# Kernel tuning notes

Hardware: AMD Instinct MI355X
Metric: run time of the kernel (lower is better)

Reference implementation:

```python
import jax, jax.numpy as jnp
import numpy as np

NUM_GROUPS, GROUP_SIZE, D_MODEL = 8, 4096, 1024
NUM_EXPERTS = 64
EXPERT_CAPACITY = 1024  # capacity_factor 2: 2 * total_tokens / num_experts


def setup_inputs() -> dict:
    key = jax.random.key(0)
    k1, k2, k3 = jax.random.split(key, 3)
    x = jax.random.normal(k1, (NUM_GROUPS, GROUP_SIZE, D_MODEL), dtype=jnp.float32)
    gate_kernel = jax.random.normal(k2, (D_MODEL, NUM_EXPERTS), dtype=jnp.float32) * 0.1
    gate_bias = jax.random.normal(k3, (NUM_EXPERTS,), dtype=jnp.float32) * 0.01
    temperature = jnp.ones((1,), dtype=jnp.float32)
    return {
        "x": x,
        "gate_kernel": gate_kernel,
        "gate_bias": gate_bias,
        "temperature": temperature,
        "expert_capacity": EXPERT_CAPACITY,
    }


def reference(x, gate_kernel, gate_bias, temperature, expert_capacity):
    # x: [G, S, D]; gate_kernel: [D, E]
    G, S, _ = x.shape
    E = gate_kernel.shape[1]

    router_logits = jnp.einsum("gsd,de->gse", x, gate_kernel) + gate_bias  # [G, S, E]
    safe_temp = jnp.maximum(temperature, 0.1)  # [1]
    router_probs = jax.nn.softmax(router_logits / safe_temp, axis=-1)  # [G, S, E]

    # Per-expert top-k over all flattened tokens.
    flat_probs = router_probs.transpose(2, 0, 1).reshape(E, G * S)  # [E, G*S]
    scores, token_indices = jax.lax.top_k(flat_probs, k=expert_capacity)  # [E, C]

    group_indices = token_indices // S  # [E, C]
    pos_indices = token_indices % S  # [E, C]
    expert_ids = jnp.broadcast_to(jnp.arange(E)[:, None], scores.shape)  # [E, C]

    # use_mask_routing=True path: scatter into capacity-limited dense masks.
    expert_masks = jnp.zeros((E, G, S), dtype=jnp.bool_).at[
        expert_ids, group_indices, pos_indices].set(True)
    weight_masks = jnp.zeros((E, G, S), dtype=x.dtype).at[
        expert_ids, group_indices, pos_indices].set(scores)

    loss = jnp.asarray(0.0, dtype=x.dtype)  # training=False
    return expert_masks, weight_masks, loss
```

## Files before the change

kernel.cpp:

```cpp
#include <hip/hip_runtime.h>
#include <math.h>

#define NG 8
#define SEQ 4096
#define DM 1024
#define NE 64
#define GS (NG * SEQ)
#define KSEL 1024
#define MASK_ELEMS (NE * GS)
#define SEG 16
#define SEGLEN (GS / SEG)
#define CAP 2048
#define CAP2 16384

typedef __attribute__((ext_vector_type(8))) short short8;
typedef __attribute__((ext_vector_type(4))) float f32x4;

__device__ __forceinline__ unsigned short f2bf(float v) {
  unsigned u = __float_as_uint(v);
  return (unsigned short)((u + 0x7FFFu + ((u >> 16) & 1u)) >> 16);
}
__device__ __forceinline__ float bf2f(unsigned short h) {
  return __uint_as_float(((unsigned)h) << 16);
}

#define GLDS(gsrc, ldst)                                                             \
  __builtin_amdgcn_global_load_lds(                                                  \
      (const __attribute__((address_space(1))) void*)(gsrc),                         \
      (__attribute__((address_space(3))) void*)(ldst), 16, 0, 0)

__global__ __launch_bounds__(256)
void k_split(const float* __restrict__ w, unsigned short* __restrict__ wph,
             unsigned short* __restrict__ wpm, unsigned* __restrict__ zbase) {
  const int t = blockIdx.x * 256 + threadIdx.x;
  if (t < NE * 256 + NE) zbase[t] = 0u;
  const int k = t >> 6, e = t & 63;
  float v = w[t];
  unsigned short h = f2bf(v); float r = v - bf2f(h);
  const int tile = k >> 5, g = (k >> 3) & 3, j = k & 7;
  const int cb = e >> 4, lrow = e & 15;
  const size_t o = (size_t)(tile * 4 + cb) * 512 + (g * 16 + lrow) * 8 + j;
  wph[o] = h; wpm[o] = f2bf(r);
}

__global__ __launch_bounds__(64)
void k_gemm_softmax(const float* __restrict__ x,
                    const unsigned short* __restrict__ wph,
                    const unsigned short* __restrict__ wpm,
                    const float* __restrict__ bias, const float* __restrict__ temp,
                    float* __restrict__ probsT) {
  __shared__ float S[8192];
  float (*Pt)[68] = (float (*)[68])S;
  float* Sf = S;

  const int lane = threadIdx.x;
  const int lrow = lane & 15, g = lane >> 4;
  const int m0 = blockIdx.x * 64;

  int irow[4], jcol[4];
  {
    union { unsigned short u[8]; short8 v; } ar, on;
#pragma unroll
    for (int j = 0; j < 8; ++j) { ar.u[j] = f2bf((float)lrow); on.u[j] = 0x3F80u; }
    f32x4 z = {0.f, 0.f, 0.f, 0.f};
    f32x4 p1 = __builtin_amdgcn_mfma_f32_16x16x32_bf16(ar.v, on.v, z, 0, 0, 0);
    f32x4 p2 = __builtin_amdgcn_mfma_f32_16x16x32_bf16(on.v, ar.v, z, 0, 0, 0);
#pragma unroll
    for (int b = 0; b < 4; ++b) {
      irow[b] = ((int)p1[b]) >> 5;
      jcol[b] = ((int)p2[b]) >> 5;
    }
  }

  f32x4 acc[4][4];
#pragma unroll
  for (int rf = 0; rf < 4; ++rf)
#pragma unroll
    for (int cb = 0; cb < 4; ++cb) acc[rf][cb] = (f32x4){0.f, 0.f, 0.f, 0.f};

#define ISSUE(T, buf)                                                                \
  {                                                                                  \
    _Pragma("unroll")                                                                \
    for (int q = 0; q < 8; ++q) {                                                    \
      const int c = q * 64 + lane;                                                   \
      const int gg = c >> 7, row = (c >> 1) & 63, half = c & 1;                      \
      const float* gsrc = x + (size_t)(m0 + row) * DM + (T) * 32 + gg * 8 + half * 4;\
      GLDS(gsrc, Sf + (buf) * 4096 + q * 256);                                       \
    }                                                                                \
    _Pragma("unroll")                                                                \
    for (int q = 0; q < 8; ++q) {                                                    \
      const unsigned short* bp = (q < 4) ? wph : wpm;                                \
      const unsigned short* gsrc = bp + (size_t)((T) * 4 + (q & 3)) * 512 + lane * 8;\
      GLDS(gsrc, Sf + (buf) * 4096 + 2048 + q * 256);                                \
    }                                                                                \
  }

#define COMPUTE(buf)                                                                 \
  {                                                                                  \
    const unsigned short* bb = (const unsigned short*)(Sf + (buf) * 4096 + 2048);    \
    _Pragma("unroll")                                                                \
    for (int rf = 0; rf < 4; ++rf) {                                                 \
      const float* ab = Sf + (buf) * 4096 + g * 512 + (rf * 16 + lrow) * 8;          \
      f32x4 lo = *(const f32x4*)ab;                                                  \
      f32x4 hi = *(const f32x4*)(ab + 4);                                            \
      union { unsigned short u[8]; short8 v; } ah, am;                               \
      _Pragma("unroll")                                                              \
      for (int j = 0; j < 8; ++j) {                                                  \
        float v0 = (j < 4) ? lo[j] : hi[j - 4];                                      \
        unsigned short h_ = f2bf(v0);                                                \
        ah.u[j] = h_; am.u[j] = f2bf(v0 - bf2f(h_));                                 \
      }                                                                              \
      _Pragma("unroll")                                                              \
      for (int cb = 0; cb < 4; ++cb) {                                               \
        short8 bh_ = *(const short8*)(bb + cb * 512 + lane * 8);                     \
        short8 bm_ = *(const short8*)(bb + 2048 + cb * 512 + lane * 8);              \
        acc[rf][cb] = __builtin_amdgcn_mfma_f32_16x16x32_bf16(ah.v, bh_,             \
                                                              acc[rf][cb], 0, 0, 0); \
        acc[rf][cb] = __builtin_amdgcn_mfma_f32_16x16x32_bf16(am.v, bh_,             \
                                                              acc[rf][cb], 0, 0, 0); \
        acc[rf][cb] = __builtin_amdgcn_mfma_f32_16x16x32_bf16(ah.v, bm_,             \
                                                              acc[rf][cb], 0, 0, 0); \
      }                                                                              \
    }                                                                                \
  }

#define WAIT16 { asm volatile("s_waitcnt vmcnt(16)" ::: "memory");                   \
                 __builtin_amdgcn_sched_barrier(0); }
#define WAIT0  { asm volatile("s_waitcnt vmcnt(0)" ::: "memory");                    \
                 __builtin_amdgcn_sched_barrier(0); }

  ISSUE(0, 0);
  ISSUE(1, 1);
  for (int t = 0; t < 30; ++t) {
    WAIT16;
    COMPUTE(t & 1);
    __builtin_amdgcn_sched_barrier(0);
    ISSUE(t + 2, t & 1);
  }
  WAIT16; COMPUTE(0);
  WAIT0;  COMPUTE(1);

#undef ISSUE
#undef COMPUTE
#undef WAIT16
#undef WAIT0

  {
    float st = temp[0];
    if (st < 0.1f) st = 0.1f;
    const float inv_t = 1.0f / st;
#pragma unroll
    for (int rf = 0; rf < 4; ++rf) {
#pragma unroll
      for (int b = 0; b < 4; ++b) {
        float l[4];
        float mx = -1.0e30f;
#pragma unroll
        for (int cb = 0; cb < 4; ++cb) {
          l[cb] = (acc[rf][cb][b] + bias[cb * 16 + jcol[b]]) * inv_t;
          mx = fmaxf(mx, l[cb]);
        }
        mx = fmaxf(mx, __shfl_xor(mx, 1));
        mx = fmaxf(mx, __shfl_xor(mx, 2));
        mx = fmaxf(mx, __shfl_xor(mx, 4));
        mx = fmaxf(mx, __shfl_xor(mx, 8));
        float p[4], s = 0.0f;
#pragma unroll
        for (int cb = 0; cb < 4; ++cb) { p[cb] = __expf(l[cb] - mx); s += p[cb]; }
        s += __shfl_xor(s, 1);
        s += __shfl_xor(s, 2);
        s += __shfl_xor(s, 4);
        s += __shfl_xor(s, 8);
        const float invs = 1.0f / s;
#pragma unroll
        for (int cb = 0; cb < 4; ++cb)
          Pt[cb * 16 + jcol[b]][rf * 16 + irow[b]] = p[cb] * invs;
      }
    }
  }

#pragma unroll
  for (int it = 0; it < 16; ++it) {
    const int e = it * 4 + (lane >> 4);
    const int tok = (lane & 15) * 4;
    *(float4*)(probsT + (size_t)e * GS + m0 + tok) = *(const float4*)(&Pt[e][tok]);
  }
}

__device__ __forceinline__ void pick_scan(const unsigned* __restrict__ bins,
                                          unsigned r_in, unsigned& bucket,
                                          unsigned& r_out, unsigned* res) {
  __syncthreads();
  const int tid = threadIdx.x;
  if (tid < 64) {
    uint4 b = ((const uint4*)bins)[tid];
    unsigned s3 = b.w, s2 = b.z + s3, s1 = b.y + s2, s0 = b.x + s1;
    unsigned suf = s0;
#pragma unroll
    for (int off = 1; off < 64; off <<= 1) {
      unsigned t = __shfl_down(suf, off);
      if (tid + off < 64) suf += t;
    }
    unsigned above = suf - s0;
    unsigned inc0 = above + s0, inc1 = above + s1, inc2 = above + s2, inc3 = above + s3;
    if (inc3 >= r_in && inc3 - b.w < r_in) { res[0] = 4 * tid + 3; res[1] = r_in - (inc3 - b.w); }
    if (inc2 >= r_in && inc2 - b.z < r_in) { res[0] = 4 * tid + 2; res[1] = r_in - (inc2 - b.z); }
    if (inc1 >= r_in && inc1 - b.y < r_in) { res[0] = 4 * tid + 1; res[1] = r_in - (inc1 - b.y); }
    if (inc0 >= r_in && inc0 - b.x < r_in) { res[0] = 4 * tid + 0; res[1] = r_in - (inc0 - b.x); }
  }
  __syncthreads();
  bucket = res[0];
  r_out = res[1];
}

__global__ __launch_bounds__(256)
void k_hist0(const float* __restrict__ probsT, unsigned* __restrict__ ghist0) {
  __shared__ unsigned h[4][256];
  const int tid = threadIdx.x, wv = tid >> 6;
  const int e = blockIdx.x >> 4;
  const int seg = blockIdx.x & (SEG - 1);
  h[0][tid] = 0; h[1][tid] = 0; h[2][tid] = 0; h[3][tid] = 0;
  __syncthreads();
  const float4* col = (const float4*)(probsT + (size_t)e * GS + seg * SEGLEN);
#pragma unroll
  for (int i = 0; i < SEGLEN / 1024; ++i) {
    float4 v = col[i * 256 + tid];
    atomicAdd(&h[wv][__float_as_uint(v.x) >> 24], 1u);
    atomicAdd(&h[wv][__float_as_uint(v.y) >> 24], 1u);
    atomicAdd(&h[wv][__float_as_uint(v.z) >> 24], 1u);
    atomicAdd(&h[wv][__float_as_uint(v.w) >> 24], 1u);
  }
  __syncthreads();
  unsigned c = h[0][tid] + h[1][tid] + h[2][tid] + h[3][tid];
  if (c) atomicAdd(&ghist0[e * 256 + tid], c);
}

__global__ __launch_bounds__(256)
void k_compact(const float* __restrict__ probsT, const unsigned* __restrict__ ghist0,
               unsigned* __restrict__ cCnt, int* __restrict__ cIdx,
               float* __restrict__ cKey) {
  __shared__ unsigned res[2];
  __shared__ unsigned locN, basePos;
  __shared__ int locIdx[2048];
  __shared__ float locKey[2048];
  const int tid = threadIdx.x;
  const int e = blockIdx.x >> 4;
  const int seg = blockIdx.x & (SEG - 1);

  if (tid == 0) locN = 0u;
  unsigned b0, r0;
  pick_scan(ghist0 + e * 256, KSEL, b0, r0, res);
  const unsigned blo = (b0 == 0u) ? 0u : (b0 - 1u);

  const float* col = probsT + (size_t)e * GS + seg * SEGLEN;
  for (int i = 0; i < SEGLEN / 256; ++i) {
    const int t = i * 256 + tid;
    const float p = col[t];
    if ((__float_as_uint(p) >> 24) >= blo) {
      unsigned pos = atomicAdd(&locN, 1u);
      locIdx[pos] = seg * SEGLEN + t;
      locKey[pos] = p;
    }
  }
  __syncthreads();
  if (tid == 0) basePos = locN ? atomicAdd(&cCnt[e], locN) : 0u;
  __syncthreads();
  const unsigned n = locN, bp = basePos;
  for (unsigned i = tid; i < n; i += 256) {
    const unsigned gp = bp + i;
    if (gp < CAP2) {
      cIdx[(size_t)e * CAP2 + gp] = locIdx[i];
      cKey[(size_t)e * CAP2 + gp] = locKey[i];
    }
  }
}

__global__ __launch_bounds__(256)
void k_select2(const unsigned* __restrict__ ghist0, const unsigned* __restrict__ cCnt,
               const int* __restrict__ cIdx, const float* __restrict__ cKey,
               const float* __restrict__ temp, unsigned* __restrict__ defCnt,
               unsigned* __restrict__ candCnt, int* __restrict__ candIdx,
               float* __restrict__ thrHiA) {
  __shared__ unsigned res[2];
  __shared__ unsigned h[4][256];
  __shared__ unsigned hs[256];
  __shared__ unsigned nd, nc;
  const int tid = threadIdx.x, wv = tid >> 6;
  const int e = blockIdx.x;
  const int cnt = (int)min(cCnt[e], (unsigned)CAP2);

  unsigned b0, r;
  pick_scan(ghist0 + e * 256, KSEL, b0, r, res);
  unsigned pfx = b0 << 24;

  for (int pass = 1; pass < 4; ++pass) {
    const int shift = 24 - 8 * pass;
    const unsigned hm = 0xFFFFFFFFu << (shift + 8);
    for (int i = tid; i < 1024; i += 256) ((unsigned*)h)[i] = 0u;
    __syncthreads();
    for (int i = tid; i < cnt; i += 256) {
      unsigned key = __float_as_uint(cKey[(size_t)e * CAP2 + i]);
      if ((key & hm) == (pfx & hm)) atomicAdd(&h[wv][(key >> shift) & 255], 1u);
    }
    __syncthreads();
    hs[tid] = h[0][tid] + h[1][tid] + h[2][tid] + h[3][tid];
    unsigned b, rn;
    pick_scan(hs, r, b, rn, res);
    pfx |= b << shift;
    r = rn;
  }

  const float thrv = __uint_as_float(pfx);
  float st = temp[0];
  if (st < 0.1f) st = 0.1f;
  const float rel = 2.0e-3f / st;
  const float hi = thrv * (1.0f + rel);
  const float lo = thrv * (1.0f - rel);
  if (tid == 0) thrHiA[e] = hi;

  if (tid == 0) { nd = 0u; nc = 0u; }
  __syncthreads();
  for (int i = tid; i < cnt; i += 256) {
    const float p = cKey[(size_t)e * CAP2 + i];
    const int t = cIdx[(size_t)e * CAP2 + i];
    if (p > hi) {
      atomicAdd(&nd, 1u);
    } else if (p >= lo) {
      unsigned pos = atomicAdd(&nc, 1u);
      if (pos < CAP) candIdx[e * CAP + pos] = t;
    }
  }
  __syncthreads();
  if (tid == 0) {
    defCnt[e] = nd;
    candCnt[e] = min(nc, (unsigned)CAP);
  }
}

__global__ __launch_bounds__(256)
void k_repair(const float* __restrict__ x, const float* __restrict__ w,
              const float* __restrict__ bias, const float* __restrict__ temp,
              const unsigned* __restrict__ candCnt, const int* __restrict__ candIdx,
              double* __restrict__ candKey) {
  __shared__ double red[4][64];
  const int e = blockIdx.x >> 4;
  const int chunk = blockIdx.x & 15;
  const int tid = threadIdx.x;
  const int ee = tid & 63, q = tid >> 6;
  const int cnt = (int)min(candCnt[e], (unsigned)CAP);

  double st = (double)temp[0];
  if (st < 0.1) st = 0.1;
  const double inv_t = 1.0 / st;

  for (int i = chunk; i < cnt; i += 16) {
    const int t = candIdx[e * CAP + i];
    const float* xr = x + (size_t)t * DM;
    double s0 = 0.0, s1 = 0.0, s2 = 0.0, s3 = 0.0;
    const int kb = q * 256;
    for (int k = kb; k < kb + 256; k += 4) {
      s0 += (double)xr[k + 0] * (double)w[(size_t)(k + 0) * NE + ee];
      s1 += (double)xr[k + 1] * (double)w[(size_t)(k + 1) * NE + ee];
      s2 += (double)xr[k + 2] * (double)w[(size_t)(k + 2) * NE + ee];
      s3 += (double)xr[k + 3] * (double)w[(size_t)(k + 3) * NE + ee];
    }
    red[q][ee] = (s0 + s1) + (s2 + s3);
    __syncthreads();
    if (tid < 64) {
      double l = (red[0][tid] + red[1][tid] + red[2][tid] + red[3][tid] +
                  (double)bias[tid]) * inv_t;
      double m = l;
#pragma unroll
      for (int off = 1; off < 64; off <<= 1) m = fmax(m, __shfl_xor(m, off));
      double ex = exp(l - m);
      double ss = ex;
#pragma unroll
      for (int off = 1; off < 64; off <<= 1) ss += __shfl_xor(ss, off);
      if (tid == e) candKey[e * CAP + i] = ex / ss;
    }
    __syncthreads();
  }
}

__global__ __launch_bounds__(256)
void k_scatter(const float* __restrict__ probsT, const float* __restrict__ thrHiA,
               float* __restrict__ out) {
  const int gid = blockIdx.x * 256 + threadIdx.x;
  const int base = gid * 4;
  const int e = base >> 15;
  float4 p = *(const float4*)(probsT + (size_t)base);
  const float hi = thrHiA[e];
  float pv[4] = {p.x, p.y, p.z, p.w};
  float mk[4], wt[4];
#pragma unroll
  for (int c = 0; c < 4; ++c) {
    bool sel = pv[c] > hi;
    mk[c] = sel ? 1.0f : 0.0f;
    wt[c] = sel ? pv[c] : 0.0f;
  }
  *(float4*)(out + (size_t)base) = make_float4(mk[0], mk[1], mk[2], mk[3]);
  *(float4*)(out + (size_t)MASK_ELEMS + base) = make_float4(wt[0], wt[1], wt[2], wt[3]);
  if (gid == 0) out[2 * (size_t)MASK_ELEMS] = 0.0f;
}

__global__ __launch_bounds__(256)
void k_finish(const unsigned* __restrict__ defCnt, const unsigned* __restrict__ candCnt,
              const int* __restrict__ candIdx, const double* __restrict__ candKey,
              const float* __restrict__ probsT, float* __restrict__ out) {
  __shared__ double kd[CAP];
  __shared__ int ti[CAP];
  const int e = blockIdx.x, tid = threadIdx.x;
  const int cnt = (int)min(candCnt[e], (unsigned)CAP);
  const int need = KSEL - (int)defCnt[e];

  for (int i = tid; i < cnt; i += 256) {
    kd[i] = candKey[e * CAP + i];
    ti[i] = candIdx[e * CAP + i];
  }
  __syncthreads();
  for (int i = tid; i < cnt; i += 256) {
    const double ki = kd[i];
    const int tii = ti[i];
    int rank = 0;
    for (int j = 0; j < cnt; ++j)
      rank += (kd[j] > ki) || (kd[j] == ki && ti[j] < tii);
    if (rank < need) {
      out[(size_t)e * GS + tii] = 1.0f;
      out[(size_t)MASK_ELEMS + (size_t)e * GS + tii] = probsT[(size_t)e * GS + tii];
    }
  }
}

extern "C" void kernel_launch(void* const* d_in, const int* in_sizes, int n_in,
                              void* d_out, int out_size, void* d_ws, size_t ws_size,
                              hipStream_t stream) {
  const float* x    = (const float*)d_in[0];
  const float* gw   = (const float*)d_in[1];
  const float* gb   = (const float*)d_in[2];
  const float* temp = (const float*)d_in[3];

  float* probsT    = (float*)d_ws;
  unsigned* ghist0 = (unsigned*)((char*)d_ws + (size_t)MASK_ELEMS * 4);
  unsigned* cCnt   = ghist0 + NE * 256;
  unsigned* defCnt = cCnt + NE;
  unsigned* candCnt = defCnt + NE;
  float* thrHiA    = (float*)(candCnt + NE);
  int* candIdx     = (int*)(thrHiA + NE);
  double* candKey  = (double*)(candIdx + NE * CAP);
  int* cIdx        = (int*)(candKey + NE * CAP);
  float* cKey      = (float*)(cIdx + (size_t)NE * CAP2);
  unsigned short* wph = (unsigned short*)(cKey + (size_t)NE * CAP2);
  unsigned short* wpm = wph + DM * NE;

  k_split<<<DM * NE / 256, 256, 0, stream>>>(gw, wph, wpm, ghist0);
  k_gemm_softmax<<<GS / 64, 64, 0, stream>>>(x, wph, wpm, gb, temp, probsT);
  k_hist0<<<NE * SEG, 256, 0, stream>>>(probsT, ghist0);
  k_compact<<<NE * SEG, 256, 0, stream>>>(probsT, ghist0, cCnt, cIdx, cKey);
  k_select2<<<NE, 256, 0, stream>>>(ghist0, cCnt, cIdx, cKey, temp, defCnt,
                                    candCnt, candIdx, thrHiA);
  k_repair<<<NE * 16, 256, 0, stream>>>(x, gw, gb, temp, candCnt, candIdx, candKey);
  k_scatter<<<MASK_ELEMS / 1024, 256, 0, stream>>>(probsT, thrHiA, (float*)d_out);
  k_finish<<<NE, 256, 0, stream>>>(defCnt, candCnt, candIdx, candKey,
                                   probsT, (float*)d_out);
}
```

Measured before the change: 112.4 us.

## Split GEMM-softmax block across four waves with XOR-swizzled K=64 staging

The router GEMM+softmax kernel moves from one 64-thread wave per 64-token block to four waves. Each wave now owns 16 rows and the cooperative loads stage a 64-wide K slice per step, which halves the pipeline iterations. The A tile in LDS uses an XOR swizzle to avoid bank conflicts, and the write-out of the transposed probabilities is shared across all 256 threads. In exchange it adds block barriers each step and doubles LDS use per block, which may reduce occupancy.

Result: faster. 92.59 us (-17.6%).

```diff
diff --git a/kernel.cpp b/kernel.cpp
--- a/kernel.cpp
+++ b/kernel.cpp
@@ -43,19 +43,21 @@
   wph[o] = h; wpm[o] = f2bf(r);
 }
 
-__global__ __launch_bounds__(64)
+__global__ __launch_bounds__(256, 2)
 void k_gemm_softmax(const float* __restrict__ x,
                     const unsigned short* __restrict__ wph,
                     const unsigned short* __restrict__ wpm,
                     const float* __restrict__ bias, const float* __restrict__ temp,
                     float* __restrict__ probsT) {
-  __shared__ float S[8192];
+  __shared__ float S[16384];
   float (*Pt)[68] = (float (*)[68])S;
-  float* Sf = S;
-
-  const int lane = threadIdx.x;
+
+  const int tid = threadIdx.x;
+  const int w = tid >> 6, lane = tid & 63;
   const int lrow = lane & 15, g = lane >> 4;
   const int m0 = blockIdx.x * 64;
+  const int arow_g = tid >> 4;
+  const int agr = (tid & 15) ^ (arow_g & 15);
 
   int irow[4], jcol[4];
   {
@@ -72,37 +74,34 @@
     }
   }
 
-  f32x4 acc[4][4];
-#pragma unroll
-  for (int rf = 0; rf < 4; ++rf)
-#pragma unroll
-    for (int cb = 0; cb < 4; ++cb) acc[rf][cb] = (f32x4){0.f, 0.f, 0.f, 0.f};
-
-#define ISSUE(T, buf)                                                                \
+  f32x4 acc[4];
+#pragma unroll
+  for (int cb = 0; cb < 4; ++cb) acc[cb] = (f32x4){0.f, 0.f, 0.f, 0.f};
+
+#define ISSUE(s, buf)                                                                \
   {                                                                                  \
     _Pragma("unroll")                                                                \
-    for (int q = 0; q < 8; ++q) {                                                    \
-      const int c = q * 64 + lane;                                                   \
-      const int gg = c >> 7, row = (c >> 1) & 63, half = c & 1;                      \
-      const float* gsrc = x + (size_t)(m0 + row) * DM + (T) * 32 + gg * 8 + half * 4;\
-      GLDS(gsrc, Sf + (buf) * 4096 + q * 256);                                       \
-    }                                                                                \
+    for (int c = 0; c < 4; ++c)                                                      \
+      GLDS(x + (size_t)(m0 + c * 16 + arow_g) * DM + (s) * 64 + agr * 4,             \
+           S + (buf) * 8192 + (c * 256 + tid) * 4);                                  \
     _Pragma("unroll")                                                                \
-    for (int q = 0; q < 8; ++q) {                                                    \
-      const unsigned short* bp = (q < 4) ? wph : wpm;                                \
-      const unsigned short* gsrc = bp + (size_t)((T) * 4 + (q & 3)) * 512 + lane * 8;\
-      GLDS(gsrc, Sf + (buf) * 4096 + 2048 + q * 256);                                \
-    }                                                                                \
+    for (int p = 0; p < 2; ++p)                                                      \
+      _Pragma("unroll")                                                              \
+      for (int c = 0; c < 2; ++c)                                                    \
+        GLDS((p ? wpm : wph) + (size_t)(s) * 4096 + c * 2048 + tid * 8,              \
+             S + (buf) * 8192 + 4096 + p * 2048 + c * 1024 + tid * 4);               \
   }
 
 #define COMPUTE(buf)                                                                 \
   {                                                                                  \
-    const unsigned short* bb = (const unsigned short*)(Sf + (buf) * 4096 + 2048);    \
+    const float* Af = S + (buf) * 8192;                                              \
+    const unsigned short* Bb = (const unsigned short*)(S + (buf) * 8192 + 4096);     \
     _Pragma("unroll")                                                                \
-    for (int rf = 0; rf < 4; ++rf) {                                                 \
-      const float* ab = Sf + (buf) * 4096 + g * 512 + (rf * 16 + lrow) * 8;          \
-      f32x4 lo = *(const f32x4*)ab;                                                  \
-      f32x4 hi = *(const f32x4*)(ab + 4);                                            \
+    for (int kt = 0; kt < 2; ++kt) {                                                 \
+      f32x4 lo = *(const f32x4*)(Af + (w * 16 + lrow) * 64 +                         \
+                                 ((kt * 8 + g * 2 + 0) ^ lrow) * 4);                 \
+      f32x4 hi = *(const f32x4*)(Af + (w * 16 + lrow) * 64 +                         \
+                                 ((kt * 8 + g * 2 + 1) ^ lrow) * 4);                 \
       union { unsigned short u[8]; short8 v; } ah, am;                               \
       _Pragma("unroll")                                                              \
       for (int j = 0; j < 8; ++j) {                                                  \
@@ -112,37 +111,38 @@
       }                                                                              \
       _Pragma("unroll")                                                              \
       for (int cb = 0; cb < 4; ++cb) {                                               \
-        short8 bh_ = *(const short8*)(bb + cb * 512 + lane * 8);                     \
-        short8 bm_ = *(const short8*)(bb + 2048 + cb * 512 + lane * 8);              \
-        acc[rf][cb] = __builtin_amdgcn_mfma_f32_16x16x32_bf16(ah.v, bh_,             \
-                                                              acc[rf][cb], 0, 0, 0); \
-        acc[rf][cb] = __builtin_amdgcn_mfma_f32_16x16x32_bf16(am.v, bh_,             \
-                                                              acc[rf][cb], 0, 0, 0); \
-        acc[rf][cb] = __builtin_amdgcn_mfma_f32_16x16x32_bf16(ah.v, bm_,             \
-                                                              acc[rf][cb], 0, 0, 0); \
+        short8 bh_ = *(const short8*)(Bb + (kt * 4 + cb) * 512 + lane * 8);          \
+        short8 bm_ = *(const short8*)(Bb + 4096 + (kt * 4 + cb) * 512 + lane * 8);   \
+        acc[cb] = __builtin_amdgcn_mfma_f32_16x16x32_bf16(ah.v, bh_, acc[cb], 0, 0, 0); \
+        acc[cb] = __builtin_amdgcn_mfma_f32_16x16x32_bf16(am.v, bh_, acc[cb], 0, 0, 0); \
+        acc[cb] = __builtin_amdgcn_mfma_f32_16x16x32_bf16(ah.v, bm_, acc[cb], 0, 0, 0); \
       }                                                                              \
     }                                                                                \
   }
 
-#define WAIT16 { asm volatile("s_waitcnt vmcnt(16)" ::: "memory");                   \
-                 __builtin_amdgcn_sched_barrier(0); }
-#define WAIT0  { asm volatile("s_waitcnt vmcnt(0)" ::: "memory");                    \
-                 __builtin_amdgcn_sched_barrier(0); }
+#define WAIT8 { asm volatile("s_waitcnt vmcnt(8)" ::: "memory");                     \
+                __builtin_amdgcn_sched_barrier(0); }
+#define WAIT0 { asm volatile("s_waitcnt vmcnt(0)" ::: "memory");                     \
+                __builtin_amdgcn_sched_barrier(0); }
 
   ISSUE(0, 0);
   ISSUE(1, 1);
-  for (int t = 0; t < 30; ++t) {
-    WAIT16;
-    COMPUTE(t & 1);
-    __builtin_amdgcn_sched_barrier(0);
-    ISSUE(t + 2, t & 1);
-  }
-  WAIT16; COMPUTE(0);
-  WAIT0;  COMPUTE(1);
+#pragma unroll
+  for (int s = 0; s < 14; ++s) {
+    WAIT8;
+    __builtin_amdgcn_s_barrier();
+    if (s & 1) { COMPUTE(1); } else { COMPUTE(0); }
+    __builtin_amdgcn_s_barrier();
+    ISSUE(s + 2, s & 1);
+  }
+  WAIT8; __builtin_amdgcn_s_barrier(); COMPUTE(0);
+  __builtin_amdgcn_s_barrier();
+  WAIT0; __builtin_amdgcn_s_barrier(); COMPUTE(1);
+  __syncthreads();
 
 #undef ISSUE
 #undef COMPUTE
-#undef WAIT16
+#undef WAIT8
 #undef WAIT0
 
   {
@@ -150,40 +150,39 @@
     if (st < 0.1f) st = 0.1f;
     const float inv_t = 1.0f / st;
 #pragma unroll
-    for (int rf = 0; rf < 4; ++rf) {
-#pragma unroll
-      for (int b = 0; b < 4; ++b) {
-        float l[4];
-        float mx = -1.0e30f;
-#pragma unroll
-        for (int cb = 0; cb < 4; ++cb) {
-          l[cb] = (acc[rf][cb][b] + bias[cb * 16 + jcol[b]]) * inv_t;
-          mx = fmaxf(mx, l[cb]);
-        }
-        mx = fmaxf(mx, __shfl_xor(mx, 1));
-        mx = fmaxf(mx, __shfl_xor(mx, 2));
-        mx = fmaxf(mx, __shfl_xor(mx, 4));
-        mx = fmaxf(mx, __shfl_xor(mx, 8));
-        float p[4], s = 0.0f;
-#pragma unroll
-        for (int cb = 0; cb < 4; ++cb) { p[cb] = __expf(l[cb] - mx); s += p[cb]; }
-        s += __shfl_xor(s, 1);
-        s += __shfl_xor(s, 2);
-        s += __shfl_xor(s, 4);
-        s += __shfl_xor(s, 8);
-        const float invs = 1.0f / s;
-#pragma unroll
-        for (int cb = 0; cb < 4; ++cb)
-          Pt[cb * 16 + jcol[b]][rf * 16 + irow[b]] = p[cb] * invs;
+    for (int b = 0; b < 4; ++b) {
+      float l[4];
+      float mx = -1.0e30f;
+#pragma unroll
+      for (int cb = 0; cb < 4; ++cb) {
+        l[cb] = (acc[cb][b] + bias[cb * 16 + jcol[b]]) * inv_t;
+        mx = fmaxf(mx, l[cb]);
       }
-    }
-  }
-
-#pragma unroll
-  for (int it = 0; it < 16; ++it) {
-    const int e = it * 4 + (lane >> 4);
-    const int tok = (lane & 15) * 4;
-    *(float4*)(probsT + (size_t)e * GS + m0 + tok) = *(const float4*)(&Pt[e][tok]);
+      mx = fmaxf(mx, __shfl_xor(mx, 1));
+      mx = fmaxf(mx, __shfl_xor(mx, 2));
+      mx = fmaxf(mx, __shfl_xor(mx, 4));
+      mx = fmaxf(mx, __shfl_xor(mx, 8));
+      float p[4], sm = 0.0f;
+#pragma unroll
+      for (int cb = 0; cb < 4; ++cb) { p[cb] = __expf(l[cb] - mx); sm += p[cb]; }
+      sm += __shfl_xor(sm, 1);
+      sm += __shfl_xor(sm, 2);
+      sm += __shfl_xor(sm, 4);
+      sm += __shfl_xor(sm, 8);
+      const float invs = 1.0f / sm;
+#pragma unroll
+      for (int cb = 0; cb < 4; ++cb)
+        Pt[cb * 16 + jcol[b]][w * 16 + irow[b]] = p[cb] * invs;
+    }
+  }
+  __syncthreads();
+
+  {
+    const int e = tid >> 2, qq = tid & 3;
+    float* dst = probsT + (size_t)e * GS + m0 + qq * 16;
+#pragma unroll
+    for (int c2 = 0; c2 < 4; ++c2)
+      *(float4*)(dst + c2 * 4) = *(const float4*)(&Pt[e][qq * 16 + c2 * 4]);
   }
 }
 
@@ -453,7 +452,7 @@
   unsigned short* wpm = wph + DM * NE;
 
   k_split<<<DM * NE / 256, 256, 0, stream>>>(gw, wph, wpm, ghist0);
-  k_gemm_softmax<<<GS / 64, 64, 0, stream>>>(x, wph, wpm, gb, temp, probsT);
+  k_gemm_softmax<<<GS / 64, 256, 0, stream>>>(x, wph, wpm, gb, temp, probsT);
   k_hist0<<<NE * SEG, 256, 0, stream>>>(probsT, ghist0);
   k_compact<<<NE * SEG, 256, 0, stream>>>(probsT, ghist0, cCnt, cIdx, cKey);
   k_select2<<<NE, 256, 0, stream>>>(ghist0, cCnt, cIdx, cKey, temp, defCnt,
```
